# Kernel tuning notes

Hardware: AMD Instinct MI355X
Metric: run time of the kernel (lower is better)

The kernel has to match this reference:

```python
import jax, jax.numpy as jnp
import numpy as np

# Loihi CUBA LIF neuron constants (netParams['neuron'])
V_TH_MANT = 80.0
THETA = V_TH_MANT * 64.0          # threshold in voltage units (vThMant << 6)
I_DECAY = 1024.0
V_DECAY = 128.0
REF_DELAY = 1.0
DECAY_U = 1.0 - I_DECAY / 4096.0  # current decay per step
DECAY_V = 1.0 - V_DECAY / 4096.0  # voltage decay per step
TAU_RHO = 1.0
SCALE_RHO = 1.0
POOL_W = 1.1 * V_TH_MANT          # SLAYER pool weight: one input spike -> 1.1*theta drive


@jax.custom_vjp
def spike_fn(v):
    # Heaviside spike with SLAYER surrogate gradient
    return (v >= THETA).astype(v.dtype)

def _spike_fwd(v):
    return spike_fn(v), v

def _spike_bwd(v, g):
    sur = (SCALE_RHO / THETA) * jnp.exp(-jnp.abs(v - THETA) / (TAU_RHO * THETA))
    return (g * sur,)

spike_fn.defvjp(_spike_fwd, _spike_bwd)


def spike_loihi(x):
    """Loihi LIF recurrence over last (time) axis. x: [..., T] weighted spikes."""
    shp = x.shape
    xt = jnp.moveaxis(x.reshape(-1, shp[-1]), -1, 0)  # [T, N]
    z = jnp.zeros(xt.shape[1], x.dtype)
    def step(carry, x_t):
        u, v, ref = carry
        u = u * DECAY_U + x_t * 64.0                  # current state (input scaled by 2^6)
        active = (ref <= 0).astype(x.dtype)
        v = (v * DECAY_V + u) * active                # voltage, clamped in refractory period
        s = spike_fn(v)
        ref = jnp.where(s > 0, REF_DELAY, jnp.maximum(ref - 1.0, 0.0))
        v = v * (1.0 - s)                             # reset on spike
        return (u, v, ref), s
    _, spikes = jax.lax.scan(step, (z, z, z), xt)
    return jnp.moveaxis(spikes, 0, -1).reshape(shp)


def delay_shift(x, d=1):
    # shift spikes forward in time by d steps (zero-pad at t=0)
    return jnp.pad(x, [(0, 0)] * (x.ndim - 1) + [(d, 0)])[..., :x.shape[-1]]


def conv2d_t(x, w):
    # x: [B,C,H,W,T], w: [O,I,k,k]; 2D 'SAME' conv applied independently per timestep
    B, C, H, W, T = x.shape
    xm = jnp.moveaxis(x, -1, 1).reshape(B * T, C, H, W)
    y = jax.lax.conv_general_dilated(xm, w, (1, 1), 'SAME',
                                     dimension_numbers=('NCHW', 'OIHW', 'NCHW'))
    O = w.shape[0]
    return jnp.moveaxis(y.reshape(B, T, O, H, W), 1, -1)


def sum_pool(x, k):
    # SLAYER pool = sum over kxk window * fixed weight (per timestep)
    y = jax.lax.reduce_window(x, 0.0, jax.lax.add,
                              (1, 1, k, k, 1), (1, 1, k, k, 1), 'VALID')
    return y * POOL_W


def setup_inputs() -> dict:
    key = jax.random.key(0)
    ks = jax.random.split(key, 5)
    B, T = 8, 128
    x = (jax.random.uniform(ks[0], (B, 2, 128, 128, T)) < 0.1).astype(jnp.float32)
    w1 = jax.random.normal(ks[1], (16, 2, 5, 5), jnp.float32) * 10.0 * 0.2   # weightScale=10
    w2 = jax.random.normal(ks[2], (32, 16, 3, 3), jnp.float32) * 50.0 * 0.2  # weightScale=50
    wf1 = jax.random.normal(ks[3], (512, 2048), jnp.float32) * 100.0 * 0.02  # dense default scale
    wf2 = jax.random.normal(ks[4], (11, 512), jnp.float32) * 100.0 * 0.02
    return {"x": x, "w1": w1, "w2": w2, "wf1": wf1, "wf2": wf2}


def reference(x, w1, w2, wf1, wf2):
    s = spike_loihi(sum_pool(x, 4))            # [B,2,32,32,T]
    s = delay_shift(s)
    s = spike_loihi(conv2d_t(s, w1))           # [B,16,32,32,T]
    s = delay_shift(s)
    s = spike_loihi(sum_pool(s, 2))            # [B,16,16,16,T]
    s = delay_shift(s)
    s = spike_loihi(conv2d_t(s, w2))           # [B,32,16,16,T]
    s = delay_shift(s)
    s = spike_loihi(sum_pool(s, 2))            # [B,32,8,8,T]
    B, T = s.shape[0], s.shape[-1]
    s = s.reshape(B, -1, T)                    # [B,2048,T]
    s = delay_shift(s)
    s = spike_loihi(jnp.einsum('bft,of->bot', s, wf1))  # [B,512,T]
    s = delay_shift(s)
    s = spike_loihi(jnp.einsum('bft,of->bot', s, wf2))  # [B,11,T]
    s = delay_shift(s)
    return s[:, :, None, None, :]              # [B,11,1,1,T]
```

## Files before the change

### kernel.cpp

```cpp
#include <hip/hip_runtime.h>

#define TT 128

#define DECAY_U 0.75f
#define DECAY_V 0.96875f
#define THETA   5120.0f
#define POOLW   88.0f

__device__ __forceinline__ void lif_step(float xt, float& u, float& v, int& refc, float& s) {
    u = __fadd_rn(__fmul_rn(u, DECAY_U), __fmul_rn(xt, 64.0f));
    float vn = __fadd_rn(__fmul_rn(v, DECAY_V), u);
    v = refc ? 0.0f : vn;
    s = (v >= THETA) ? 1.0f : 0.0f;
    if (s > 0.f) { refc = 1; v = 0.f; }
    else         { refc = refc > 0 ? refc - 1 : 0; }
}

__device__ __forceinline__ void lif_seq_lds(float* col, int stride) {
    float u = 0.f, v = 0.f;
    int refc = 0;
    #pragma unroll 16
    for (int t = 0; t < TT; ++t) {
        float s;
        lif_step(col[t * stride], u, v, refc, s);
        col[t * stride] = s;
    }
}

__global__ void lut_build_k(const float* __restrict__ w1, const float* __restrict__ w2,
                            float* __restrict__ LUT1, float* __restrict__ LUT2) {
    int id = blockIdx.x * 256 + threadIdx.x;
    if (id < 81920) {
        int ky = id >> 14;
        int idx = (id >> 4) & 1023;
        int oc = id & 15;
        float s = 0.f;
        #pragma unroll
        for (int j = 0; j < 10; ++j)
            if ((idx >> j) & 1) {
                int kx = j >> 1, c = j & 1;
                s += w1[oc*50 + c*25 + ky*5 + kx];
            }
        LUT1[id] = s;
    }
    if (id < 147456) {
        int th = id >> 13;
        int idx = (id >> 5) & 255;
        int oc = id & 31;
        int tap = th >> 1, half = th & 1;
        float s = 0.f;
        #pragma unroll
        for (int j = 0; j < 8; ++j)
            if ((idx >> j) & 1)
                s += w2[oc*144 + (half*8 + j)*9 + tap];
        LUT2[id] = s;
    }
}

__global__ void pool1_lif_k(const float* __restrict__ x, unsigned char* __restrict__ pk1) {
    __shared__ float sb[TT][3];
    int t = threadIdx.x & 127, c = threadIdx.x >> 7;
    int pos = blockIdx.x & 1023, b = blockIdx.x >> 10;
    int px = pos & 31, py = pos >> 5;
    const float* base = x + (size_t)((((b*2 + c)*128 + py*4)*128) + px*4) * 128 + t;
    float s = 0.f;
    #pragma unroll
    for (int dy = 0; dy < 4; ++dy)
        #pragma unroll
        for (int dx = 0; dx < 4; ++dx)
            s += base[(dy*128 + dx) * 128];
    sb[t][c] = s * POOLW;
    __syncthreads();
    if (threadIdx.x < 2) lif_seq_lds(&sb[0][threadIdx.x], 3);
    __syncthreads();
    if (threadIdx.x < 128) {
        unsigned int v = (sb[t][0] > 0.5f ? 1u : 0u) | (sb[t][1] > 0.5f ? 2u : 0u);
        pk1[(size_t)b * 131072 + (size_t)pos * 128 + t] = (unsigned char)v;
    }
}

__global__ __launch_bounds__(128) void conv1_lut_k(const unsigned char* __restrict__ pk1,
                                                   const float* __restrict__ LUT1,
                                                   unsigned short* __restrict__ pk2) {
    __shared__ float sb[TT*17];
    int t = threadIdx.x;
    int pos = blockIdx.x & 1023, b = blockIdx.x >> 10;
    int px = pos & 31, py = pos >> 5;
    const unsigned char* pp = pk1 + (size_t)b * 131072;

    unsigned int idx[5];
    #pragma unroll
    for (int ky = 0; ky < 5; ++ky) {
        int iy = py + ky - 2;
        unsigned int v = 0;
        #pragma unroll
        for (int kx = 0; kx < 5; ++kx) {
            int ix = px + kx - 2;
            bool vs = ((unsigned)iy < 32u) && ((unsigned)ix < 32u) && (t > 0);
            unsigned int nb = vs ? (unsigned int)pp[(iy*32 + ix)*128 + t - 1] : 0u;
            v |= nb << (kx*2);
        }
        idx[ky] = v;
    }

    float acc[16];
    #pragma unroll
    for (int k = 0; k < 16; ++k) acc[k] = 0.f;
    #pragma unroll
    for (int ky = 0; ky < 5; ++ky) {
        const float4* Lp = (const float4*)(LUT1 + (size_t)(ky*1024 + idx[ky]) * 16);
        #pragma unroll
        for (int q = 0; q < 4; ++q) {
            float4 l = Lp[q];
            acc[q*4+0] += l.x;
            acc[q*4+1] += l.y;
            acc[q*4+2] += l.z;
            acc[q*4+3] += l.w;
        }
    }

    #pragma unroll
    for (int oc = 0; oc < 16; ++oc) sb[t*17 + oc] = acc[oc];
    __syncthreads();
    if (t < 16) lif_seq_lds(&sb[t], 17);
    __syncthreads();
    {
        unsigned int w = 0;
        #pragma unroll
        for (int oc = 0; oc < 16; ++oc)
            w |= (sb[t*17 + oc] > 0.5f ? 1u : 0u) << oc;
        pk2[(size_t)b * 131072 + (size_t)pos * 128 + t] = (unsigned short)w;
    }
}

__global__ __launch_bounds__(256) void pool2pack_k(const unsigned short* __restrict__ pk2,
                                                   unsigned short* __restrict__ pk3) {
    __shared__ float sb[TT][17];
    int tid = threadIdx.x;
    int t = tid & 127, half = tid >> 7;
    int pos = blockIdx.x & 255, b = blockIdx.x >> 8;
    int px = pos & 15, py = pos >> 4;
    unsigned int w0 = 0, w1 = 0, w2 = 0, w3 = 0;
    if (t > 0) {
        const unsigned short* q = pk2 + (size_t)b * 131072 + (size_t)(py*2*32 + px*2) * 128 + (t - 1);
        w0 = q[0]; w1 = q[128]; w2 = q[32*128]; w3 = q[33*128];
    }
    #pragma unroll
    for (int j = 0; j < 8; ++j) {
        int c = half*8 + j;
        int cnt = ((w0 >> c) & 1) + ((w1 >> c) & 1) + ((w2 >> c) & 1) + ((w3 >> c) & 1);
        sb[t][c] = POOLW * (float)cnt;
    }
    __syncthreads();
    if (tid < 16) lif_seq_lds(&sb[0][tid], 17);
    __syncthreads();
    if (tid < 128) {
        unsigned int w = 0;
        #pragma unroll
        for (int c = 0; c < 16; ++c)
            w |= (sb[tid][c] > 0.5f ? 1u : 0u) << c;
        pk3[(size_t)b * 32768 + (size_t)pos * 128 + tid] = (unsigned short)w;
    }
}

__global__ __launch_bounds__(128) void conv2_lut_k(const unsigned short* __restrict__ pk3,
                                                   const float* __restrict__ LUT2,
                                                   unsigned int* __restrict__ pk4) {
    __shared__ float sb[TT*33];
    int t = threadIdx.x;
    int pos = blockIdx.x & 255, b = blockIdx.x >> 8;
    int px = pos & 15, py = pos >> 4;
    const unsigned short* pp = pk3 + (size_t)b * 32768;

    unsigned int wv[9];
    #pragma unroll
    for (int tap = 0; tap < 9; ++tap) {
        int ky = tap / 3, kx = tap - ky*3;
        int iy = py + ky - 1, ix = px + kx - 1;
        bool vs = ((unsigned)iy < 16u) && ((unsigned)ix < 16u) && (t > 0);
        wv[tap] = vs ? (unsigned int)pp[(iy*16 + ix)*128 + t - 1] : 0u;
    }

    float acc[32];
    #pragma unroll
    for (int k = 0; k < 32; ++k) acc[k] = 0.f;
    #pragma unroll
    for (int tap = 0; tap < 9; ++tap) {
        const float4* p0 = (const float4*)(LUT2 + (size_t)((tap*2 + 0)*256 + (wv[tap] & 255u)) * 32);
        #pragma unroll
        for (int q = 0; q < 8; ++q) {
            float4 l = p0[q];
            acc[q*4+0] += l.x;
            acc[q*4+1] += l.y;
            acc[q*4+2] += l.z;
            acc[q*4+3] += l.w;
        }
        const float4* p1 = (const float4*)(LUT2 + (size_t)((tap*2 + 1)*256 + ((wv[tap] >> 8) & 255u)) * 32);
        #pragma unroll
        for (int q = 0; q < 8; ++q) {
            float4 l = p1[q];
            acc[q*4+0] += l.x;
            acc[q*4+1] += l.y;
            acc[q*4+2] += l.z;
            acc[q*4+3] += l.w;
        }
    }

    #pragma unroll
    for (int oc = 0; oc < 32; ++oc) sb[t*33 + oc] = acc[oc];
    __syncthreads();
    if (t < 32) lif_seq_lds(&sb[t], 33);
    __syncthreads();
    {
        unsigned int w = 0;
        #pragma unroll
        for (int oc = 0; oc < 32; ++oc)
            w |= (sb[t*33 + oc] > 0.5f ? 1u : 0u) << oc;
        pk4[(size_t)b * 32768 + (size_t)pos * 128 + t] = w;
    }
}

__global__ void pool3_lif_k(const unsigned int* __restrict__ pk4, float* __restrict__ s5) {
    __shared__ float sb[TT][3];
    int t = threadIdx.x & 127, pos = threadIdx.x >> 7;
    int n = blockIdx.x * 2 + pos;
    int px = n & 7, py = (n >> 3) & 7, c = (n >> 6) & 31, b = n >> 11;
    float acc = 0.f;
    if (t > 0) {
        const unsigned int* q = pk4 + (size_t)b * 32768 + (size_t)(py*2*16 + px*2) * 128 + (t - 1);
        unsigned int w0 = q[0], w1 = q[128], w2 = q[16*128], w3 = q[17*128];
        int cnt = ((w0 >> c) & 1) + ((w1 >> c) & 1) + ((w2 >> c) & 1) + ((w3 >> c) & 1);
        acc = POOLW * (float)cnt;
    }
    sb[t][pos] = acc;
    __syncthreads();
    if (threadIdx.x < 2) lif_seq_lds(&sb[0][threadIdx.x], 3);
    __syncthreads();
    s5[(size_t)n * TT + t] = sb[t][pos];
}

__global__ __launch_bounds__(256) void fc1_gemm_k(const float* __restrict__ s5,
                                                  const float* __restrict__ wf1,
                                                  float* __restrict__ part) {
    __shared__ float WT[64][68];
    __shared__ float ST[64][68];
    int bid = blockIdx.x;
    int kc = bid & 7;
    int ot = (bid >> 3) & 7;
    int tt = (bid >> 6) & 1;
    int b  = bid >> 7;
    int tid = threadIdx.x;
    int oo = tid >> 4;
    int to = tid & 15;

    const float* wbase = wf1 + (size_t)(ot*64) * 2048 + kc*256;
    const float* sbase = s5 + (size_t)b * 262144 + (size_t)(kc*256) * 128;

    float acc[4][4];
    #pragma unroll
    for (int i = 0; i < 4; ++i)
        #pragma unroll
        for (int j = 0; j < 4; ++j) acc[i][j] = 0.f;

    for (int ks = 0; ks < 4; ++ks) {
        __syncthreads();
        #pragma unroll
        for (int i = 0; i < 16; ++i) {
            int e = tid + 256*i;
            int o = e >> 6, f = e & 63;
            WT[f][o] = wbase[(size_t)o * 2048 + ks*64 + f];
        }
        #pragma unroll
        for (int i = 0; i < 16; ++i) {
            int e = tid + 256*i;
            int f = e >> 6, tl = e & 63;
            int tsrc = tt*64 + tl - 1;
            ST[f][tl] = (tsrc < 0) ? 0.f : sbase[(size_t)f * 128 + ks*64*128 + tsrc];
        }
        __syncthreads();
        #pragma unroll 4
        for (int k = 0; k < 64; ++k) {
            float4 a = *(const float4*)&WT[k][oo*4];
            float4 s = *(const float4*)&ST[k][to*4];
            acc[0][0] = fmaf(a.x, s.x, acc[0][0]);
            acc[0][1] = fmaf(a.x, s.y, acc[0][1]);
            acc[0][2] = fmaf(a.x, s.z, acc[0][2]);
            acc[0][3] = fmaf(a.x, s.w, acc[0][3]);
            acc[1][0] = fmaf(a.y, s.x, acc[1][0]);
            acc[1][1] = fmaf(a.y, s.y, acc[1][1]);
            acc[1][2] = fmaf(a.y, s.z, acc[1][2]);
            acc[1][3] = fmaf(a.y, s.w, acc[1][3]);
            acc[2][0] = fmaf(a.z, s.x, acc[2][0]);
            acc[2][1] = fmaf(a.z, s.y, acc[2][1]);
            acc[2][2] = fmaf(a.z, s.z, acc[2][2]);
            acc[2][3] = fmaf(a.z, s.w, acc[2][3]);
            acc[3][0] = fmaf(a.w, s.x, acc[3][0]);
            acc[3][1] = fmaf(a.w, s.y, acc[3][1]);
            acc[3][2] = fmaf(a.w, s.z, acc[3][2]);
            acc[3][3] = fmaf(a.w, s.w, acc[3][3]);
        }
    }
    float* pb = part + (size_t)kc * 524288 + (size_t)b * 65536
              + (size_t)(ot*64 + oo*4) * 128 + tt*64 + to*4;
    #pragma unroll
    for (int i = 0; i < 4; ++i)
        #pragma unroll
        for (int j = 0; j < 4; ++j)
            pb[(size_t)i * 128 + j] = acc[i][j];
}

__global__ void fc1_reduce_lif_k(const float* __restrict__ part, float* __restrict__ s6) {
    __shared__ float sb[TT][3];
    int t = threadIdx.x & 127, pos = threadIdx.x >> 7;
    int n = blockIdx.x * 2 + pos;
    float s = 0.f;
    #pragma unroll
    for (int kc = 0; kc < 8; ++kc)
        s += part[(size_t)kc * 524288 + (size_t)n * 128 + t];
    sb[t][pos] = s;
    __syncthreads();
    if (threadIdx.x < 2) lif_seq_lds(&sb[0][threadIdx.x], 3);
    __syncthreads();
    s6[(size_t)n * TT + t] = sb[t][pos];
}

__global__ void fc2_lif_k(const float* __restrict__ s6, const float* __restrict__ wf2,
                          float* __restrict__ out) {
    __shared__ float sb[TT];
    int t = threadIdx.x;
    int o = blockIdx.x % 11, b = blockIdx.x / 11;
    float acc = 0.f;
    if (t > 0) {
        const float* sp = s6 + (size_t)b * 65536 + (t - 1);
        const float* wp = wf2 + o * 512;
        for (int f = 0; f < 512; f += 4) {
            float4 w = *(const float4*)&wp[f];
            acc = fmaf(w.x, sp[(size_t)f * 128], acc);
            acc = fmaf(w.y, sp[(size_t)(f+1) * 128], acc);
            acc = fmaf(w.z, sp[(size_t)(f+2) * 128], acc);
            acc = fmaf(w.w, sp[(size_t)(f+3) * 128], acc);
        }
    }
    sb[t] = acc;
    __syncthreads();
    if (t == 0) lif_seq_lds(sb, 1);
    __syncthreads();
    float* q = out + (size_t)(b*11 + o) * TT;
    if (t == 0) q[0] = 0.f;
    if (t < TT - 1) q[t + 1] = sb[t];
}

extern "C" void kernel_launch(void* const* d_in, const int* in_sizes, int n_in,
                              void* d_out, int out_size, void* d_ws, size_t ws_size,
                              hipStream_t stream) {
    const float* x   = (const float*)d_in[0];
    const float* w1  = (const float*)d_in[1];
    const float* w2  = (const float*)d_in[2];
    const float* wf1 = (const float*)d_in[3];
    const float* wf2 = (const float*)d_in[4];
    float* out = (float*)d_out;

    float* ws = (float*)d_ws;
    float* PART = ws;
    float* A    = PART + 4194304;
    float* S6   = A + 2097152;
    float* LUT1 = S6 + 524288;
    float* LUT2 = LUT1 + 81920;
    unsigned char*  PK1 = (unsigned char*)(LUT2 + 147456);
    unsigned short* PK2 = (unsigned short*)(PK1 + 1048576);
    unsigned short* PK3 = (unsigned short*)((char*)PK2 + 2097152);
    unsigned int*   PK4 = (unsigned int*)((char*)PK3 + 524288);

    lut_build_k<<<dim3(576), 256, 0, stream>>>(w1, w2, LUT1, LUT2);
    pool1_lif_k<<<dim3(8192), 256, 0, stream>>>(x, PK1);
    conv1_lut_k<<<dim3(8192), 128, 0, stream>>>(PK1, LUT1, PK2);
    pool2pack_k<<<dim3(2048), 256, 0, stream>>>(PK2, PK3);
    conv2_lut_k<<<dim3(2048), 128, 0, stream>>>(PK3, LUT2, PK4);
    pool3_lif_k<<<dim3(8192), 256, 0, stream>>>(PK4, A);
    fc1_gemm_k      <<<dim3(1024), 256, 0, stream>>>(A, wf1, PART);
    fc1_reduce_lif_k<<<dim3(2048), 256, 0, stream>>>(PART, S6);
    fc2_lif_k<<<dim3(88), 128, 0, stream>>>(S6, wf2, out);
}
```

Measured before the change: 205.9 us.

## Parallelize conv LUT accumulation over output channels with shared-memory index staging

The conv1 and conv2 LUT kernels now use 256 threads per block. The packed neighbourhood indices are gathered once into shared memory, and the LUT accumulation is split so each thread handles one output channel for a group of timesteps. Previously each thread accumulated all 16 or 32 channels with float4 loads. The change is meant to cut per-thread register pressure and spread the LUT gather across more threads, at the cost of scalar instead of vector loads and an extra barrier.

```diff
diff --git a/kernel.cpp b/kernel.cpp
--- a/kernel.cpp
+++ b/kernel.cpp
@@ -79,56 +79,54 @@
     }
 }
 
-__global__ __launch_bounds__(128) void conv1_lut_k(const unsigned char* __restrict__ pk1,
+__global__ __launch_bounds__(256) void conv1_lut_k(const unsigned char* __restrict__ pk1,
                                                    const float* __restrict__ LUT1,
                                                    unsigned short* __restrict__ pk2) {
+    __shared__ unsigned int XIDX[5*132];
     __shared__ float sb[TT*17];
-    int t = threadIdx.x;
+    int tid = threadIdx.x;
     int pos = blockIdx.x & 1023, b = blockIdx.x >> 10;
     int px = pos & 31, py = pos >> 5;
     const unsigned char* pp = pk1 + (size_t)b * 131072;
 
-    unsigned int idx[5];
-    #pragma unroll
-    for (int ky = 0; ky < 5; ++ky) {
-        int iy = py + ky - 2;
-        unsigned int v = 0;
-        #pragma unroll
-        for (int kx = 0; kx < 5; ++kx) {
-            int ix = px + kx - 2;
-            bool vs = ((unsigned)iy < 32u) && ((unsigned)ix < 32u) && (t > 0);
-            unsigned int nb = vs ? (unsigned int)pp[(iy*32 + ix)*128 + t - 1] : 0u;
-            v |= nb << (kx*2);
-        }
-        idx[ky] = v;
-    }
-
-    float acc[16];
-    #pragma unroll
-    for (int k = 0; k < 16; ++k) acc[k] = 0.f;
-    #pragma unroll
-    for (int ky = 0; ky < 5; ++ky) {
-        const float4* Lp = (const float4*)(LUT1 + (size_t)(ky*1024 + idx[ky]) * 16);
-        #pragma unroll
-        for (int q = 0; q < 4; ++q) {
-            float4 l = Lp[q];
-            acc[q*4+0] += l.x;
-            acc[q*4+1] += l.y;
-            acc[q*4+2] += l.z;
-            acc[q*4+3] += l.w;
-        }
-    }
-
-    #pragma unroll
-    for (int oc = 0; oc < 16; ++oc) sb[t*17 + oc] = acc[oc];
-    __syncthreads();
-    if (t < 16) lif_seq_lds(&sb[t], 17);
-    __syncthreads();
-    {
+    #pragma unroll
+    for (int i = 0; i < 3; ++i) {
+        int e = tid + 256*i;
+        if (e < 640) {
+            int ky = e >> 7, t = e & 127;
+            int iy = py + ky - 2;
+            unsigned int v = 0;
+            #pragma unroll
+            for (int kx = 0; kx < 5; ++kx) {
+                int ix = px + kx - 2;
+                bool vs = ((unsigned)iy < 32u) && ((unsigned)ix < 32u) && (t > 0);
+                unsigned int nb = vs ? (unsigned int)pp[(iy*32 + ix)*128 + t - 1] : 0u;
+                v |= nb << (kx*2);
+            }
+            XIDX[ky*132 + t] = v;
+        }
+    }
+    __syncthreads();
+
+    int oc = tid & 15, tg = tid >> 4;
+    #pragma unroll
+    for (int i = 0; i < 8; ++i) {
+        int t = tg*8 + i;
+        float acc = 0.f;
+        #pragma unroll
+        for (int ky = 0; ky < 5; ++ky)
+            acc += LUT1[(size_t)(ky*1024 + XIDX[ky*132 + t]) * 16 + oc];
+        sb[t*17 + oc] = acc;
+    }
+    __syncthreads();
+    if (tid < 16) lif_seq_lds(&sb[tid], 17);
+    __syncthreads();
+    if (tid < 128) {
+        int t = tid;
         unsigned int w = 0;
         #pragma unroll
-        for (int oc = 0; oc < 16; ++oc)
-            w |= (sb[t*17 + oc] > 0.5f ? 1u : 0u) << oc;
+        for (int o = 0; o < 16; ++o)
+            w |= (sb[t*17 + o] > 0.5f ? 1u : 0u) << o;
         pk2[(size_t)b * 131072 + (size_t)pos * 128 + t] = (unsigned short)w;
     }
 }
@@ -163,59 +161,51 @@
     }
 }
 
-__global__ __launch_bounds__(128) void conv2_lut_k(const unsigned short* __restrict__ pk3,
+__global__ __launch_bounds__(256) void conv2_lut_k(const unsigned short* __restrict__ pk3,
                                                    const float* __restrict__ LUT2,
                                                    unsigned int* __restrict__ pk4) {
+    __shared__ unsigned int XL[9*132];
     __shared__ float sb[TT*33];
-    int t = threadIdx.x;
+    int tid = threadIdx.x;
     int pos = blockIdx.x & 255, b = blockIdx.x >> 8;
     int px = pos & 15, py = pos >> 4;
     const unsigned short* pp = pk3 + (size_t)b * 32768;
 
-    unsigned int wv[9];
-    #pragma unroll
-    for (int tap = 0; tap < 9; ++tap) {
-        int ky = tap / 3, kx = tap - ky*3;
-        int iy = py + ky - 1, ix = px + kx - 1;
-        bool vs = ((unsigned)iy < 16u) && ((unsigned)ix < 16u) && (t > 0);
-        wv[tap] = vs ? (unsigned int)pp[(iy*16 + ix)*128 + t - 1] : 0u;
-    }
-
-    float acc[32];
-    #pragma unroll
-    for (int k = 0; k < 32; ++k) acc[k] = 0.f;
-    #pragma unroll
-    for (int tap = 0; tap < 9; ++tap) {
-        const float4* p0 = (const float4*)(LUT2 + (size_t)((tap*2 + 0)*256 + (wv[tap] & 255u)) * 32);
-        #pragma unroll
-        for (int q = 0; q < 8; ++q) {
-            float4 l = p0[q];
-            acc[q*4+0] += l.x;
-            acc[q*4+1] += l.y;
-            acc[q*4+2] += l.z;
-            acc[q*4+3] += l.w;
-        }
-        const float4* p1 = (const float4*)(LUT2 + (size_t)((tap*2 + 1)*256 + ((wv[tap] >> 8) & 255u)) * 32);
-        #pragma unroll
-        for (int q = 0; q < 8; ++q) {
-            float4 l = p1[q];
-            acc[q*4+0] += l.x;
-            acc[q*4+1] += l.y;
-            acc[q*4+2] += l.z;
-            acc[q*4+3] += l.w;
-        }
-    }
-
-    #pragma unroll
-    for (int oc = 0; oc < 32; ++oc) sb[t*33 + oc] = acc[oc];
-    __syncthreads();
-    if (t < 32) lif_seq_lds(&sb[t], 33);
-    __syncthreads();
-    {
+    #pragma unroll
+    for (int i = 0; i < 5; ++i) {
+        int e = tid + 256*i;
+        if (e < 1152) {
+            int tap = e >> 7, t = e & 127;
+            int ky = tap / 3, kx = tap - ky*3;
+            int iy = py + ky - 1, ix = px + kx - 1;
+            bool vs = ((unsigned)iy < 16u) && ((unsigned)ix < 16u) && (t > 0);
+            XL[tap*132 + t] = vs ? (unsigned int)pp[(iy*16 + ix)*128 + t - 1] : 0u;
+        }
+    }
+    __syncthreads();
+
+    int oc = tid & 31, tg = tid >> 5;
+    #pragma unroll 1
+    for (int i = 0; i < 16; ++i) {
+        int t = tg*16 + i;
+        float acc = 0.f;
+        #pragma unroll
+        for (int tap = 0; tap < 9; ++tap) {
+            unsigned int w = XL[tap*132 + t];
+            acc += LUT2[(size_t)((tap*2 + 0)*256 + (w & 255u)) * 32 + oc];
+            acc += LUT2[(size_t)((tap*2 + 1)*256 + ((w >> 8) & 255u)) * 32 + oc];
+        }
+        sb[t*33 + oc] = acc;
+    }
+    __syncthreads();
+    if (tid < 32) lif_seq_lds(&sb[tid], 33);
+    __syncthreads();
+    if (tid < 128) {
+        int t = tid;
         unsigned int w = 0;
         #pragma unroll
-        for (int oc = 0; oc < 32; ++oc)
-            w |= (sb[t*33 + oc] > 0.5f ? 1u : 0u) << oc;
+        for (int o = 0; o < 32; ++o)
+            w |= (sb[t*33 + o] > 0.5f ? 1u : 0u) << o;
         pk4[(size_t)b * 32768 + (size_t)pos * 128 + t] = w;
     }
 }
@@ -373,9 +363,9 @@
 
     lut_build_k<<<dim3(576), 256, 0, stream>>>(w1, w2, LUT1, LUT2);
     pool1_lif_k<<<dim3(8192), 256, 0, stream>>>(x, PK1);
-    conv1_lut_k<<<dim3(8192), 128, 0, stream>>>(PK1, LUT1, PK2);
+    conv1_lut_k<<<dim3(8192), 256, 0, stream>>>(PK1, LUT1, PK2);
     pool2pack_k<<<dim3(2048), 256, 0, stream>>>(PK2, PK3);
-    conv2_lut_k<<<dim3(2048), 128, 0, stream>>>(PK3, LUT2, PK4);
+    conv2_lut_k<<<dim3(2048), 256, 0, stream>>>(PK3, LUT2, PK4);
     pool3_lif_k<<<dim3(8192), 256, 0, stream>>>(PK4, A);
     fc1_gemm_k      <<<dim3(1024), 256, 0, stream>>>(A, wf1, PART);
     fc1_reduce_lif_k<<<dim3(2048), 256, 0, stream>>>(PART, S6);
```

After: 199.1 us, median of 2. 3.3% less time.
